# Kernel optimization log

Hardware: AMD Instinct MI355X
Metric: run time of the kernel (lower is better)

## Reference

```python
import jax, jax.numpy as jnp
import numpy as np

S, E, H = 4096, 1024, 16
D = E // H
N_SEG = 64


def setup_inputs() -> dict:
    key = jax.random.key(0)
    ks = jax.random.split(key, 11)
    scale = 0.02
    inp = {
        "x": jax.random.normal(ks[0], (S, E), dtype=jnp.float32),
        "Wq": jax.random.normal(ks[1], (E, E), dtype=jnp.float32) * scale,
        "bq": jax.random.normal(ks[2], (E,), dtype=jnp.float32) * scale,
        "Wk": jax.random.normal(ks[3], (E, E), dtype=jnp.float32) * scale,
        "bk": jax.random.normal(ks[4], (E,), dtype=jnp.float32) * scale,
        "Wv": jax.random.normal(ks[5], (E, E), dtype=jnp.float32) * scale,
        "bv": jax.random.normal(ks[6], (E,), dtype=jnp.float32) * scale,
        "Wo": jax.random.normal(ks[7], (E, E), dtype=jnp.float32) * scale,
        "bo": jax.random.normal(ks[8], (E,), dtype=jnp.float32) * scale,
        "segment_ids": jnp.sort(jax.random.randint(ks[9], (S,), 0, N_SEG)).astype(jnp.int32),
        "pos": 100,
    }
    return inp


def reference(x, Wq, bq, Wk, bk, Wv, bv, Wo, bo, segment_ids, pos):
    # torch Linear: y = x @ W.T + b
    q = (x @ Wq.T + bq).reshape(S, H, D)  # [S, H, D]
    k = (x @ Wk.T + bk).reshape(S, H, D)
    v = (x @ Wv.T + bv).reshape(S, H, D)

    # same-segment mask (contiguous segments from gene-structure dividers)
    mask = segment_ids[:, None] == segment_ids[None, :]  # [S, S]

    # NOTE: original leaves out-of-segment scores at 0 (not -inf) and applies
    # softmax over the FULL row; also no 1/sqrt(d) scaling. Reproduce exactly.
    scores = jnp.einsum("shd,thd->hst", q, k)            # [H, S, S]
    scores = jnp.where(mask[None, :, :], scores, 0.0)
    weights = jax.nn.softmax(scores, axis=-1)            # softmax over full row

    wv = jnp.einsum("hst,thd->shd", weights, v).reshape(S, E)
    out = wv @ Wo.T + bo                                  # [S, E]

    # mean over the main context: tokens sharing pos's segment
    main = (segment_ids == segment_ids[pos]).astype(out.dtype)  # [S]
    result = (out * main[:, None]).sum(axis=0) / main.sum()
    return result
```

## Files before the change

### kernel.cpp

```cpp
#include <hip/hip_runtime.h>
#include <math.h>

#define SS 4096
#define EE 1024
#define HH 16
#define DD 64
#define RMAX 128
#define NCOL 128
#define NTR  8
#define NRED 8
#define NPROJ 768
#define NBG 64
#define NVS 16
#define NATT 256

#define OFF_SUMX  64
#define OFF_BGA   1088
#define OFF_BETA  2112
#define OFF_ALPHA 3136
#define OFF_VSUM  3200
#define OFF_PART  8192
#define OFF_XT    (OFF_PART + EE * NCOL)
#define OFF_QH    (OFF_XT + EE * RMAX)
#define OFF_KTH   (OFF_QH + HH * RMAX * DD)
#define OFF_VH    (OFF_KTH + HH * DD * RMAX)

__device__ __forceinline__ void seg_scan(const int* __restrict__ seg,
                                         const int* __restrict__ posp,
                                         int* sh, int& s0, int& L) {
    if (threadIdx.x == 0) { sh[0] = SS; sh[1] = -1; }
    __syncthreads();
    int sid = seg[posp[0]];
    int lmin = SS, lmax = -1;
    for (int i = threadIdx.x; i < SS; i += 256)
        if (seg[i] == sid) { lmin = min(lmin, i); lmax = max(lmax, i); }
#pragma unroll
    for (int off = 32; off; off >>= 1) {
        lmin = min(lmin, __shfl_xor(lmin, off));
        lmax = max(lmax, __shfl_xor(lmax, off));
    }
    if ((threadIdx.x & 63) == 0) { atomicMin(&sh[0], lmin); atomicMax(&sh[1], lmax); }
    __syncthreads();
    s0 = sh[0];
    L  = sh[1] - sh[0] + 1;
    if (L > RMAX) L = RMAX;
    if (L < 1)    L = 1;
}

__global__ __launch_bounds__(256) void d0_kernel(
    const float* __restrict__ x, const int* __restrict__ seg,
    const int* __restrict__ posp, float* __restrict__ ws) {
    int bid = blockIdx.x, tid = threadIdx.x;
    if (bid < NCOL) {
        float* partT = ws + OFF_PART;
        int r0 = bid * (SS / NCOL);
        const float4* x4 = (const float4*)x;
        float4 a = make_float4(0.f, 0.f, 0.f, 0.f);
#pragma unroll 8
        for (int r = 0; r < SS / NCOL; ++r) {
            float4 v = x4[(size_t)(r0 + r) * 256 + tid];
            a.x += v.x; a.y += v.y; a.z += v.z; a.w += v.w;
        }
        partT[(size_t)(4 * tid + 0) * NCOL + bid] = a.x;
        partT[(size_t)(4 * tid + 1) * NCOL + bid] = a.y;
        partT[(size_t)(4 * tid + 2) * NCOL + bid] = a.z;
        partT[(size_t)(4 * tid + 3) * NCOL + bid] = a.w;
        return;
    }
    __shared__ float t[128 * 129];
    __shared__ int sh[2];
    int s0, L;
    seg_scan(seg, posp, sh, s0, L);
    int kb = bid - NCOL;
    if (kb == 0 && tid == 0) { ((int*)ws)[0] = s0; ((int*)ws)[1] = L; }
    int k0 = kb * 128;
    float* xT = ws + OFF_XT;
    for (int idx = tid; idx < 128 * 32; idx += 256) {
        int r = idx >> 5, c4 = idx & 31;
        float4 v = make_float4(0.f, 0.f, 0.f, 0.f);
        if (r < L) v = *(const float4*)(x + (size_t)(s0 + r) * EE + k0 + c4 * 4);
        t[r * 129 + c4 * 4 + 0] = v.x;
        t[r * 129 + c4 * 4 + 1] = v.y;
        t[r * 129 + c4 * 4 + 2] = v.z;
        t[r * 129 + c4 * 4 + 3] = v.w;
    }
    __syncthreads();
    for (int idx = tid; idx < 128 * 32; idx += 256) {
        int k = idx >> 5, r4 = idx & 31;
        float4 o;
        o.x = t[(r4 * 4 + 0) * 129 + k];
        o.y = t[(r4 * 4 + 1) * 129 + k];
        o.z = t[(r4 * 4 + 2) * 129 + k];
        o.w = t[(r4 * 4 + 3) * 129 + k];
        *(float4*)(xT + (size_t)(k0 + k) * RMAX + r4 * 4) = o;
    }
}

__global__ __launch_bounds__(256) void d1_kernel(
    const float* __restrict__ Wq, const float* __restrict__ bq,
    const float* __restrict__ Wk, const float* __restrict__ bk,
    const float* __restrict__ Wv, const float* __restrict__ bv,
    float* __restrict__ ws) {
    int bid = blockIdx.x, tid = threadIdx.x;
    if (bid < NRED) {
        if (bid == 0) {
            for (int i = tid; i < 1088; i += 256) (ws + OFF_BETA)[i] = 0.f;
        }
        const float* partT = ws + OFF_PART;
        int e  = bid * 128 + (tid >> 1);
        int c0 = (tid & 1) * 64;
        const float4* p4 = (const float4*)(partT + (size_t)e * NCOL + c0);
        float4 s4 = make_float4(0.f, 0.f, 0.f, 0.f);
#pragma unroll
        for (int i = 0; i < 16; ++i) {
            float4 v = p4[i];
            s4.x += v.x; s4.y += v.y; s4.z += v.z; s4.w += v.w;
        }
        float s = s4.x + s4.y + s4.z + s4.w;
        s += __shfl_xor(s, 1);
        if ((tid & 1) == 0) (ws + OFF_SUMX)[e] = s;
        return;
    }
    __shared__ float wsL[4 * EE];
    __shared__ float red[16 * 66];
    int L  = ((const int*)ws)[1];
    int Lp = (L + 63) & ~63;
    int nh = Lp >> 6;
    int pid = bid - NRED;
    int m   = pid >> 8;
    int eb  = pid & 255;
    int e0  = eb * 4;
    const float* W = (m == 0) ? Wq : ((m == 1) ? Wk : Wv);
    const float* b = (m == 0) ? bq : ((m == 1) ? bk : bv);

    {
        const float4* src = (const float4*)(W + (size_t)e0 * EE);
        float4* dst = (float4*)wsL;
#pragma unroll
        for (int i = 0; i < 4; ++i) dst[tid + i * 256] = src[tid + i * 256];
    }
    __syncthreads();

    int lane = tid & 63;
    int w4   = tid >> 6;
    int kbase = w4 * 256;
    const float* x0 = ws + OFF_XT + lane;
    float acc[2][4] = {{0.f, 0.f, 0.f, 0.f}, {0.f, 0.f, 0.f, 0.f}};
    for (int kk = 0; kk < 256; kk += 8) {
        float xv0[8], xv1[8];
#pragma unroll
        for (int u = 0; u < 8; ++u)
            xv0[u] = x0[(size_t)(kbase + kk + u) * RMAX];
        if (nh == 2) {
#pragma unroll
            for (int u = 0; u < 8; ++u)
                xv1[u] = x0[(size_t)(kbase + kk + u) * RMAX + 64];
        }
#pragma unroll
        for (int j = 0; j < 4; ++j) {
            const float4* wp = (const float4*)&wsL[j * EE + kbase + kk];
            float4 wa = wp[0], wb = wp[1];
            acc[0][j] += wa.x * xv0[0] + wa.y * xv0[1] + wa.z * xv0[2] + wa.w * xv0[3]
                       + wb.x * xv0[4] + wb.y * xv0[5] + wb.z * xv0[6] + wb.w * xv0[7];
            if (nh == 2)
                acc[1][j] += wa.x * xv1[0] + wa.y * xv1[1] + wa.z * xv1[2] + wa.w * xv1[3]
                           + wb.x * xv1[4] + wb.y * xv1[5] + wb.z * xv1[6] + wb.w * xv1[7];
        }
    }

    float* qh  = ws + OFF_QH;
    float* kTh = ws + OFF_KTH;
    float* vh  = ws + OFF_VH;
    int h = e0 >> 6;
    for (int h2 = 0; h2 < nh; ++h2) {
        __syncthreads();
#pragma unroll
        for (int j = 0; j < 4; ++j)
            red[(w4 * 4 + j) * 66 + lane] = acc[h2][j];
        __syncthreads();
        int p  = w4;
        int rg = h2 * 64 + lane;
        float v = 0.f;
        if (rg < L)
            v = red[(0 * 4 + p) * 66 + lane] + red[(1 * 4 + p) * 66 + lane]
              + red[(2 * 4 + p) * 66 + lane] + red[(3 * 4 + p) * 66 + lane]
              + b[e0 + p];
        int d0 = (e0 & 63) + p;
        if (m == 1) kTh[(size_t)(h * DD + d0) * RMAX + rg] = v;
        else        ((m == 0) ? qh : vh)[((size_t)h * RMAX + rg) * DD + d0] = v;
    }
}

__global__ __launch_bounds__(256) void d2_kernel(
    const float* __restrict__ Wv, const float* __restrict__ bv,
    float* __restrict__ ws) {
    __shared__ float qS[4 * 64];
    __shared__ float wS[4 * 128];
    __shared__ float vp_[4][64];
    const float* sumx = ws + OFF_SUMX;
    float* bgA    = ws + OFF_BGA;
    float* betap  = ws + OFF_BETA;
    float* alphap = ws + OFF_ALPHA;
    float* vsumh  = ws + OFF_VSUM;
    const float* qh  = ws + OFF_QH;
    const float* kTh = ws + OFF_KTH;
    const float* vh  = ws + OFF_VH;

    int bid = blockIdx.x, tid = threadIdx.x;
    int lane = tid & 63, wave = tid >> 6;
    int L  = ((const int*)ws)[1];
    int Lp = (L + 63) & ~63;

    if (bid < NBG) {
        int e = bid * 16 + (tid >> 4);
        int j = tid & 15;
        const float4* wr  = (const float4*)(Wv + (size_t)e * EE);
        const float4* sx4 = (const float4*)sumx;
        float p = 0.f;
#pragma unroll
        for (int jj = 0; jj < 16; ++jj) {
            float4 w = wr[jj * 16 + j], z = sx4[jj * 16 + j];
            p += w.x * z.x + w.y * z.y + w.z * z.z + w.w * z.w;
        }
        p += __shfl_xor(p, 8);
        p += __shfl_xor(p, 4);
        p += __shfl_xor(p, 2);
        p += __shfl_xor(p, 1);
        if (j == 0) bgA[e] = p + (float)SS * bv[e];
        return;
    }
    if (bid < NBG + NVS) {
        int h = bid - NBG;
        float s = 0.f;
        for (int t = wave; t < Lp; t += 4)
            s += vh[((size_t)h * RMAX + t) * DD + lane];
        vp_[wave][lane] = s;
        __syncthreads();
        if (wave == 0)
            vsumh[h * DD + lane] = vp_[0][lane] + vp_[1][lane]
                                 + vp_[2][lane] + vp_[3][lane];
        return;
    }

    int aid = bid - NBG - NVS;
    int gidbase = aid * 4 + wave;
    int pairs = L * HH;
    float* qSw = qS + wave * 64;
    float* wSw = wS + wave * 128;
    for (int wg = gidbase; wg < pairs; wg += NATT * 4) {
        int h = wg & (HH - 1);
        int r = wg >> 4;
        qSw[lane] = qh[((size_t)h * RMAX + r) * DD + lane];
        float s0 = 0.f, s1 = 0.f;
#pragma unroll
        for (int d = 0; d < 64; ++d) {
            float qd = qSw[d];
            const float* kr = kTh + (size_t)(h * DD + d) * RMAX;
            s0 += qd * kr[lane];
            s1 += qd * kr[64 + lane];
        }
        float v0 = (lane < L)      ? s0 : -3.0e38f;
        float v1 = (64 + lane < L) ? s1 : -3.0e38f;
        float m = fmaxf(0.f, fmaxf(v0, v1));
#pragma unroll
        for (int off = 32; off; off >>= 1) m = fmaxf(m, __shfl_xor(m, off));
        float w0 = (lane < L)      ? __expf(s0 - m) : 0.f;
        float w1 = (64 + lane < L) ? __expf(s1 - m) : 0.f;
        float Zl = w0 + w1;
#pragma unroll
        for (int off = 32; off; off >>= 1) Zl += __shfl_xor(Zl, off);
        float em = __expf(-m);
        float Z  = Zl + (float)(SS - L) * em;
        wSw[lane]      = w0;
        wSw[64 + lane] = w1;
        float acc = 0.f;
#pragma unroll 16
        for (int t = 0; t < Lp; ++t)
            acc += wSw[t] * vh[((size_t)h * RMAX + t) * DD + lane];
        float invZ = 1.0f / Z;
        atomicAdd(&betap[h * DD + lane], acc * invZ);
        if (lane == 0) atomicAdd(&alphap[h], em * invZ);
    }
}

__global__ __launch_bounds__(256) void d3_kernel(
    const float* __restrict__ Wo, const float* __restrict__ bo,
    const float* __restrict__ ws, float* __restrict__ out) {
    __shared__ float z[EE];
    int tid = threadIdx.x;
    int lane = tid & 63, wave = tid >> 6;
    int L = ((const int*)ws)[1];

    {
        int h = tid >> 4;
        float4 beta = ((const float4*)(ws + OFF_BETA))[tid];
        float  a    = (ws + OFF_ALPHA)[h];
        float4 g    = ((const float4*)(ws + OFF_BGA))[tid];
        float4 vs   = ((const float4*)(ws + OFF_VSUM))[tid];
        ((float4*)z)[tid] = make_float4(beta.x + a * (g.x - vs.x),
                                        beta.y + a * (g.y - vs.y),
                                        beta.z + a * (g.z - vs.z),
                                        beta.w + a * (g.w - vs.w));
    }
    __syncthreads();

    int e = blockIdx.x * 4 + wave;
    const float4* wr = (const float4*)(Wo + (size_t)e * EE);
    const float4* z4 = (const float4*)z;
    float p = 0.f;
#pragma unroll
    for (int it = 0; it < 4; ++it) {
        float4 w = wr[it * 64 + lane], zz = z4[it * 64 + lane];
        p += w.x * zz.x + w.y * zz.y + w.z * zz.z + w.w * zz.w;
    }
#pragma unroll
    for (int off = 32; off; off >>= 1) p += __shfl_xor(p, off);
    if (lane == 0) out[e] = bo[e] + p / (float)L;
}

extern "C" void kernel_launch(void* const* d_in, const int* in_sizes, int n_in,
                              void* d_out, int out_size, void* d_ws, size_t ws_size,
                              hipStream_t stream) {
    const float* x   = (const float*)d_in[0];
    const float* Wq  = (const float*)d_in[1];
    const float* bq  = (const float*)d_in[2];
    const float* Wk  = (const float*)d_in[3];
    const float* bk  = (const float*)d_in[4];
    const float* Wv  = (const float*)d_in[5];
    const float* bv  = (const float*)d_in[6];
    const float* Wo  = (const float*)d_in[7];
    const float* bo  = (const float*)d_in[8];
    const int*   seg = (const int*)d_in[9];
    const int*   pos = (const int*)d_in[10];
    float*       out = (float*)d_out;
    float*       ws  = (float*)d_ws;

    d0_kernel<<<NCOL + NTR, 256, 0, stream>>>(x, seg, pos, ws);
    d1_kernel<<<NRED + NPROJ, 256, 0, stream>>>(Wq, bq, Wk, bk, Wv, bv, ws);
    d2_kernel<<<NBG + NVS + NATT, 256, 0, stream>>>(Wv, bv, ws);
    d3_kernel<<<EE / 4, 256, 0, stream>>>(Wo, bo, ws, out);
}
```

Baseline: 71.57 us.

## Tile QKV projection over rows/cols with split-K partials and separate reduce kernel

Drops the separate transpose of the main-segment rows of x. The QKV projection kernel now loads x rows and W tiles straight into shared memory, computing 64-row by 32-column tiles split four ways over K, and writes partial sums to workspace. A new d1b kernel adds the four partials plus bias and scatters the results into the per-head q, kT and v layouts. This trades the old per-block full-K reduction and x-transpose pass for more parallel blocks and smaller W tiles, at the cost of an extra kernel launch and a round trip of the partial sums through global memory.

```diff
diff --git a/kernel.cpp b/kernel.cpp
--- a/kernel.cpp
+++ b/kernel.cpp
@@ -7,9 +7,9 @@
 #define DD 64
 #define RMAX 128
 #define NCOL 128
-#define NTR  8
 #define NRED 8
 #define NPROJ 768
+#define NREDB 96
 #define NBG 64
 #define NVS 16
 #define NATT 256
@@ -20,10 +20,10 @@
 #define OFF_ALPHA 3136
 #define OFF_VSUM  3200
 #define OFF_PART  8192
-#define OFF_XT    (OFF_PART + EE * NCOL)
-#define OFF_QH    (OFF_XT + EE * RMAX)
+#define OFF_QH    270336
 #define OFF_KTH   (OFF_QH + HH * RMAX * DD)
 #define OFF_VH    (OFF_KTH + HH * DD * RMAX)
+#define OFF_YP    (OFF_VH + HH * RMAX * DD)
 
 __device__ __forceinline__ void seg_scan(const int* __restrict__ seg,
                                          const int* __restrict__ posp,
@@ -67,40 +67,16 @@
         partT[(size_t)(4 * tid + 3) * NCOL + bid] = a.w;
         return;
     }
-    __shared__ float t[128 * 129];
     __shared__ int sh[2];
     int s0, L;
     seg_scan(seg, posp, sh, s0, L);
-    int kb = bid - NCOL;
-    if (kb == 0 && tid == 0) { ((int*)ws)[0] = s0; ((int*)ws)[1] = L; }
-    int k0 = kb * 128;
-    float* xT = ws + OFF_XT;
-    for (int idx = tid; idx < 128 * 32; idx += 256) {
-        int r = idx >> 5, c4 = idx & 31;
-        float4 v = make_float4(0.f, 0.f, 0.f, 0.f);
-        if (r < L) v = *(const float4*)(x + (size_t)(s0 + r) * EE + k0 + c4 * 4);
-        t[r * 129 + c4 * 4 + 0] = v.x;
-        t[r * 129 + c4 * 4 + 1] = v.y;
-        t[r * 129 + c4 * 4 + 2] = v.z;
-        t[r * 129 + c4 * 4 + 3] = v.w;
-    }
-    __syncthreads();
-    for (int idx = tid; idx < 128 * 32; idx += 256) {
-        int k = idx >> 5, r4 = idx & 31;
-        float4 o;
-        o.x = t[(r4 * 4 + 0) * 129 + k];
-        o.y = t[(r4 * 4 + 1) * 129 + k];
-        o.z = t[(r4 * 4 + 2) * 129 + k];
-        o.w = t[(r4 * 4 + 3) * 129 + k];
-        *(float4*)(xT + (size_t)(k0 + k) * RMAX + r4 * 4) = o;
-    }
+    if (tid == 0) { ((int*)ws)[0] = s0; ((int*)ws)[1] = L; }
 }
 
 __global__ __launch_bounds__(256) void d1_kernel(
-    const float* __restrict__ Wq, const float* __restrict__ bq,
-    const float* __restrict__ Wk, const float* __restrict__ bk,
-    const float* __restrict__ Wv, const float* __restrict__ bv,
-    float* __restrict__ ws) {
+    const float* __restrict__ x,
+    const float* __restrict__ Wq, const float* __restrict__ Wk,
+    const float* __restrict__ Wv, float* __restrict__ ws) {
     int bid = blockIdx.x, tid = threadIdx.x;
     if (bid < NRED) {
         if (bid == 0) {
@@ -121,73 +97,110 @@
         if ((tid & 1) == 0) (ws + OFF_SUMX)[e] = s;
         return;
     }
-    __shared__ float wsL[4 * EE];
-    __shared__ float red[16 * 66];
+    __shared__ float xs[64 * 130];
+    __shared__ float wsm[128 * 36];
+    int s0 = ((const int*)ws)[0];
     int L  = ((const int*)ws)[1];
     int Lp = (L + 63) & ~63;
-    int nh = Lp >> 6;
     int pid = bid - NRED;
-    int m   = pid >> 8;
-    int eb  = pid & 255;
-    int e0  = eb * 4;
+    int rt  = (pid >= 384) ? 1 : 0;
+    int rem = pid - rt * 384;
+    int m   = rem >> 7;
+    int rem2 = rem & 127;
+    int kc  = rem2 >> 5;
+    int et  = rem2 & 31;
+    int r0  = rt * 64;
+    if (r0 >= Lp) return;
     const float* W = (m == 0) ? Wq : ((m == 1) ? Wk : Wv);
-    const float* b = (m == 0) ? bq : ((m == 1) ? bk : bv);
-
-    {
-        const float4* src = (const float4*)(W + (size_t)e0 * EE);
-        float4* dst = (float4*)wsL;
-#pragma unroll
-        for (int i = 0; i < 4; ++i) dst[tid + i * 256] = src[tid + i * 256];
-    }
-    __syncthreads();
-
+    int e0t = et * 32;
     int lane = tid & 63;
     int w4   = tid >> 6;
-    int kbase = w4 * 256;
-    const float* x0 = ws + OFF_XT + lane;
-    float acc[2][4] = {{0.f, 0.f, 0.f, 0.f}, {0.f, 0.f, 0.f, 0.f}};
-    for (int kk = 0; kk < 256; kk += 8) {
-        float xv0[8], xv1[8];
-#pragma unroll
-        for (int u = 0; u < 8; ++u)
-            xv0[u] = x0[(size_t)(kbase + kk + u) * RMAX];
-        if (nh == 2) {
-#pragma unroll
-            for (int u = 0; u < 8; ++u)
-                xv1[u] = x0[(size_t)(kbase + kk + u) * RMAX + 64];
-        }
-#pragma unroll
-        for (int j = 0; j < 4; ++j) {
-            const float4* wp = (const float4*)&wsL[j * EE + kbase + kk];
-            float4 wa = wp[0], wb = wp[1];
-            acc[0][j] += wa.x * xv0[0] + wa.y * xv0[1] + wa.z * xv0[2] + wa.w * xv0[3]
-                       + wb.x * xv0[4] + wb.y * xv0[5] + wb.z * xv0[6] + wb.w * xv0[7];
-            if (nh == 2)
-                acc[1][j] += wa.x * xv1[0] + wa.y * xv1[1] + wa.z * xv1[2] + wa.w * xv1[3]
-                           + wb.x * xv1[4] + wb.y * xv1[5] + wb.z * xv1[6] + wb.w * xv1[7];
-        }
-    }
-
+    int eo   = w4 * 8;
+    float a0 = 0.f, a1 = 0.f, a2 = 0.f, a3 = 0.f;
+    float a4 = 0.f, a5 = 0.f, a6 = 0.f, a7 = 0.f;
+
+    for (int rr = 0; rr < 2; ++rr) {
+        int k0 = kc * 256 + rr * 128;
+        __syncthreads();
+        for (int idx = tid; idx < 2048; idx += 256) {
+            int k4 = idx & 31, r = idx >> 5;
+            float4 v = make_float4(0.f, 0.f, 0.f, 0.f);
+            if (r0 + r < L)
+                v = *(const float4*)(x + (size_t)(s0 + r0 + r) * EE + k0 + k4 * 4);
+            int kb = k4 * 2;
+            xs[(kb + 0) * 130 + r * 2 + 0] = v.x;
+            xs[(kb + 0) * 130 + r * 2 + 1] = v.y;
+            xs[(kb + 1) * 130 + r * 2 + 0] = v.z;
+            xs[(kb + 1) * 130 + r * 2 + 1] = v.w;
+        }
+        for (int idx = tid; idx < 1024; idx += 256) {
+            int k4 = idx & 31, e = idx >> 5;
+            float4 v = *(const float4*)(W + (size_t)(e0t + e) * EE + k0 + k4 * 4);
+            wsm[(k4 * 4 + 0) * 36 + e] = v.x;
+            wsm[(k4 * 4 + 1) * 36 + e] = v.y;
+            wsm[(k4 * 4 + 2) * 36 + e] = v.z;
+            wsm[(k4 * 4 + 3) * 36 + e] = v.w;
+        }
+        __syncthreads();
+#pragma unroll 8
+        for (int k2 = 0; k2 < 64; ++k2) {
+            float2 xr = *(const float2*)&xs[k2 * 130 + lane * 2];
+            const float4* wA = (const float4*)&wsm[(2 * k2 + 0) * 36 + eo];
+            const float4* wB = (const float4*)&wsm[(2 * k2 + 1) * 36 + eo];
+            float4 wa0 = wA[0], wa1 = wA[1];
+            float4 wb0 = wB[0], wb1 = wB[1];
+            a0 += wa0.x * xr.x + wb0.x * xr.y;
+            a1 += wa0.y * xr.x + wb0.y * xr.y;
+            a2 += wa0.z * xr.x + wb0.z * xr.y;
+            a3 += wa0.w * xr.x + wb0.w * xr.y;
+            a4 += wa1.x * xr.x + wb1.x * xr.y;
+            a5 += wa1.y * xr.x + wb1.y * xr.y;
+            a6 += wa1.z * xr.x + wb1.z * xr.y;
+            a7 += wa1.w * xr.x + wb1.w * xr.y;
+        }
+    }
+    float* dst = ws + OFF_YP + ((size_t)(m * 4 + kc) * RMAX + (r0 + lane)) * EE
+               + e0t + eo;
+    *(float4*)(dst)     = make_float4(a0, a1, a2, a3);
+    *(float4*)(dst + 4) = make_float4(a4, a5, a6, a7);
+}
+
+__global__ __launch_bounds__(256) void d1b_kernel(
+    const float* __restrict__ bq, const float* __restrict__ bk,
+    const float* __restrict__ bv, float* __restrict__ ws) {
+    int bid = blockIdx.x, tid = threadIdx.x;
+    int L = ((const int*)ws)[1];
+    int m  = bid / 32;
+    int rg = bid % 32;
+    const float* b = (m == 0) ? bq : ((m == 1) ? bk : bv);
     float* qh  = ws + OFF_QH;
     float* kTh = ws + OFF_KTH;
     float* vh  = ws + OFF_VH;
-    int h = e0 >> 6;
-    for (int h2 = 0; h2 < nh; ++h2) {
-        __syncthreads();
-#pragma unroll
-        for (int j = 0; j < 4; ++j)
-            red[(w4 * 4 + j) * 66 + lane] = acc[h2][j];
-        __syncthreads();
-        int p  = w4;
-        int rg = h2 * 64 + lane;
-        float v = 0.f;
-        if (rg < L)
-            v = red[(0 * 4 + p) * 66 + lane] + red[(1 * 4 + p) * 66 + lane]
-              + red[(2 * 4 + p) * 66 + lane] + red[(3 * 4 + p) * 66 + lane]
-              + b[e0 + p];
-        int d0 = (e0 & 63) + p;
-        if (m == 1) kTh[(size_t)(h * DD + d0) * RMAX + rg] = v;
-        else        ((m == 0) ? qh : vh)[((size_t)h * RMAX + rg) * DD + d0] = v;
+    float4 bb = ((const float4*)b)[tid];
+    int e = tid * 4;
+    int h = e >> 6, d = e & 63;
+#pragma unroll
+    for (int rr = 0; rr < 4; ++rr) {
+        int r = rg * 4 + rr;
+        const float4* y0 = (const float4*)(ws + OFF_YP + ((size_t)(m * 4 + 0) * RMAX + r) * EE);
+        const float4* y1 = (const float4*)(ws + OFF_YP + ((size_t)(m * 4 + 1) * RMAX + r) * EE);
+        const float4* y2 = (const float4*)(ws + OFF_YP + ((size_t)(m * 4 + 2) * RMAX + r) * EE);
+        const float4* y3 = (const float4*)(ws + OFF_YP + ((size_t)(m * 4 + 3) * RMAX + r) * EE);
+        float4 s0 = y0[tid], s1 = y1[tid], s2 = y2[tid], s3 = y3[tid];
+        float o0 = s0.x + s1.x + s2.x + s3.x + bb.x;
+        float o1 = s0.y + s1.y + s2.y + s3.y + bb.y;
+        float o2 = s0.z + s1.z + s2.z + s3.z + bb.z;
+        float o3 = s0.w + s1.w + s2.w + s3.w + bb.w;
+        if (r >= L) { o0 = 0.f; o1 = 0.f; o2 = 0.f; o3 = 0.f; }
+        if (m == 1) {
+            kTh[(size_t)(h * DD + d + 0) * RMAX + r] = o0;
+            kTh[(size_t)(h * DD + d + 1) * RMAX + r] = o1;
+            kTh[(size_t)(h * DD + d + 2) * RMAX + r] = o2;
+            kTh[(size_t)(h * DD + d + 3) * RMAX + r] = o3;
+        } else {
+            float* y = (m == 0) ? qh : vh;
+            *(float4*)&y[((size_t)h * RMAX + r) * DD + d] = make_float4(o0, o1, o2, o3);
+        }
     }
 }
 
@@ -335,8 +348,9 @@
     float*       out = (float*)d_out;
     float*       ws  = (float*)d_ws;
 
-    d0_kernel<<<NCOL + NTR, 256, 0, stream>>>(x, seg, pos, ws);
-    d1_kernel<<<NRED + NPROJ, 256, 0, stream>>>(Wq, bq, Wk, bk, Wv, bv, ws);
+    d0_kernel<<<NCOL + 1, 256, 0, stream>>>(x, seg, pos, ws);
+    d1_kernel<<<NRED + NPROJ, 256, 0, stream>>>(x, Wq, Wk, Wv, ws);
+    d1b_kernel<<<NREDB, 256, 0, stream>>>(bq, bk, bv, ws);
     d2_kernel<<<NBG + NVS + NATT, 256, 0, stream>>>(Wv, bv, ws);
     d3_kernel<<<EE / 4, 256, 0, stream>>>(Wo, bo, ws, out);
 }
```

Measured after the change: 71.50 us. No clear change (-0.1%).

## Drop x transpose stage; project QKV with register-held weight rows and shuffle reduction

Applied to the files above, without the earlier changes.

Removes the d0 transpose blocks that wrote a transposed copy of the main-segment rows of x into workspace. The QKV projection now keeps each output column's weight row in registers, split across 32 lanes, and streams x rows straight from global memory. Each row's dot product is reduced with wavefront shuffles, and the next row is double-buffered in registers. This cuts the transpose pass, the workspace round-trip and the LDS staging, at the cost of a serial per-row shuffle reduction and only 384 projection blocks.

```diff
diff --git a/kernel.cpp b/kernel.cpp
--- a/kernel.cpp
+++ b/kernel.cpp
@@ -7,9 +7,8 @@
 #define DD 64
 #define RMAX 128
 #define NCOL 128
-#define NTR  8
 #define NRED 8
-#define NPROJ 768
+#define NPROJ 384
 #define NBG 64
 #define NVS 16
 #define NATT 256
@@ -20,8 +19,7 @@
 #define OFF_ALPHA 3136
 #define OFF_VSUM  3200
 #define OFF_PART  8192
-#define OFF_XT    (OFF_PART + EE * NCOL)
-#define OFF_QH    (OFF_XT + EE * RMAX)
+#define OFF_QH    270336
 #define OFF_KTH   (OFF_QH + HH * RMAX * DD)
 #define OFF_VH    (OFF_KTH + HH * DD * RMAX)
 
@@ -67,36 +65,14 @@
         partT[(size_t)(4 * tid + 3) * NCOL + bid] = a.w;
         return;
     }
-    __shared__ float t[128 * 129];
     __shared__ int sh[2];
     int s0, L;
     seg_scan(seg, posp, sh, s0, L);
-    int kb = bid - NCOL;
-    if (kb == 0 && tid == 0) { ((int*)ws)[0] = s0; ((int*)ws)[1] = L; }
-    int k0 = kb * 128;
-    float* xT = ws + OFF_XT;
-    for (int idx = tid; idx < 128 * 32; idx += 256) {
-        int r = idx >> 5, c4 = idx & 31;
-        float4 v = make_float4(0.f, 0.f, 0.f, 0.f);
-        if (r < L) v = *(const float4*)(x + (size_t)(s0 + r) * EE + k0 + c4 * 4);
-        t[r * 129 + c4 * 4 + 0] = v.x;
-        t[r * 129 + c4 * 4 + 1] = v.y;
-        t[r * 129 + c4 * 4 + 2] = v.z;
-        t[r * 129 + c4 * 4 + 3] = v.w;
-    }
-    __syncthreads();
-    for (int idx = tid; idx < 128 * 32; idx += 256) {
-        int k = idx >> 5, r4 = idx & 31;
-        float4 o;
-        o.x = t[(r4 * 4 + 0) * 129 + k];
-        o.y = t[(r4 * 4 + 1) * 129 + k];
-        o.z = t[(r4 * 4 + 2) * 129 + k];
-        o.w = t[(r4 * 4 + 3) * 129 + k];
-        *(float4*)(xT + (size_t)(k0 + k) * RMAX + r4 * 4) = o;
-    }
+    if (tid == 0) { ((int*)ws)[0] = s0; ((int*)ws)[1] = L; }
 }
 
 __global__ __launch_bounds__(256) void d1_kernel(
+    const float* __restrict__ x,
     const float* __restrict__ Wq, const float* __restrict__ bq,
     const float* __restrict__ Wk, const float* __restrict__ bk,
     const float* __restrict__ Wv, const float* __restrict__ bv,
@@ -121,74 +97,71 @@
         if ((tid & 1) == 0) (ws + OFF_SUMX)[e] = s;
         return;
     }
-    __shared__ float wsL[4 * EE];
-    __shared__ float red[16 * 66];
+    int s0 = ((const int*)ws)[0];
     int L  = ((const int*)ws)[1];
     int Lp = (L + 63) & ~63;
-    int nh = Lp >> 6;
-    int pid = bid - NRED;
-    int m   = pid >> 8;
-    int eb  = pid & 255;
-    int e0  = eb * 4;
-    const float* W = (m == 0) ? Wq : ((m == 1) ? Wk : Wv);
-    const float* b = (m == 0) ? bq : ((m == 1) ? bk : bv);
-
-    {
-        const float4* src = (const float4*)(W + (size_t)e0 * EE);
-        float4* dst = (float4*)wsL;
-#pragma unroll
-        for (int i = 0; i < 4; ++i) dst[tid + i * 256] = src[tid + i * 256];
-    }
-    __syncthreads();
-
+    int pid  = bid - NRED;
     int lane = tid & 63;
     int w4   = tid >> 6;
-    int kbase = w4 * 256;
-    const float* x0 = ws + OFF_XT + lane;
-    float acc[2][4] = {{0.f, 0.f, 0.f, 0.f}, {0.f, 0.f, 0.f, 0.f}};
-    for (int kk = 0; kk < 256; kk += 8) {
-        float xv0[8], xv1[8];
-#pragma unroll
-        for (int u = 0; u < 8; ++u)
-            xv0[u] = x0[(size_t)(kbase + kk + u) * RMAX];
-        if (nh == 2) {
-#pragma unroll
-            for (int u = 0; u < 8; ++u)
-                xv1[u] = x0[(size_t)(kbase + kk + u) * RMAX + 64];
-        }
-#pragma unroll
-        for (int j = 0; j < 4; ++j) {
-            const float4* wp = (const float4*)&wsL[j * EE + kbase + kk];
-            float4 wa = wp[0], wb = wp[1];
-            acc[0][j] += wa.x * xv0[0] + wa.y * xv0[1] + wa.z * xv0[2] + wa.w * xv0[3]
-                       + wb.x * xv0[4] + wb.y * xv0[5] + wb.z * xv0[6] + wb.w * xv0[7];
-            if (nh == 2)
-                acc[1][j] += wa.x * xv1[0] + wa.y * xv1[1] + wa.z * xv1[2] + wa.w * xv1[3]
-                           + wb.x * xv1[4] + wb.y * xv1[5] + wb.z * xv1[6] + wb.w * xv1[7];
-        }
-    }
-
+    int e2   = lane >> 5;
+    int kg   = lane & 31;
+    int ge   = pid * 8 + w4 * 2 + e2;
+    int m    = ge >> 10;
+    int em   = ge & 1023;
+    const float* Wm = (m == 0) ? Wq : ((m == 1) ? Wk : Wv);
+    const float* bm = (m == 0) ? bq : ((m == 1) ? bk : bv);
+    float bias = bm[em];
+    const float4* wp = (const float4*)(Wm + (size_t)em * EE + kg * 32);
+    float4 w0 = wp[0], w1 = wp[1], w2 = wp[2], w3 = wp[3];
+    float4 w4v = wp[4], w5 = wp[5], w6 = wp[6], w7 = wp[7];
+    int h = em >> 6, d = em & 63;
     float* qh  = ws + OFF_QH;
     float* kTh = ws + OFF_KTH;
     float* vh  = ws + OFF_VH;
-    int h = e0 >> 6;
-    for (int h2 = 0; h2 < nh; ++h2) {
-        __syncthreads();
-#pragma unroll
-        for (int j = 0; j < 4; ++j)
-            red[(w4 * 4 + j) * 66 + lane] = acc[h2][j];
-        __syncthreads();
-        int p  = w4;
-        int rg = h2 * 64 + lane;
-        float v = 0.f;
-        if (rg < L)
-            v = red[(0 * 4 + p) * 66 + lane] + red[(1 * 4 + p) * 66 + lane]
-              + red[(2 * 4 + p) * 66 + lane] + red[(3 * 4 + p) * 66 + lane]
-              + b[e0 + p];
-        int d0 = (e0 & 63) + p;
-        if (m == 1) kTh[(size_t)(h * DD + d0) * RMAX + rg] = v;
-        else        ((m == 0) ? qh : vh)[((size_t)h * RMAX + rg) * DD + d0] = v;
-    }
+    int r0off = pid & (Lp - 1);
+
+#define LOADX(A0,A1,A2,A3,A4,A5,A6,A7, RR)                                   \
+    {                                                                         \
+        int r_  = (r0off + (RR)) & (Lp - 1);                                  \
+        int rx_ = (r_ < L) ? (s0 + r_) : s0;                                  \
+        const float4* xp_ = (const float4*)(x + (size_t)rx_ * EE + kg * 32);  \
+        A0 = xp_[0]; A1 = xp_[1]; A2 = xp_[2]; A3 = xp_[3];                   \
+        A4 = xp_[4]; A5 = xp_[5]; A6 = xp_[6]; A7 = xp_[7];                   \
+    }
+#define BODY(A0,A1,A2,A3,A4,A5,A6,A7, RR)                                    \
+    {                                                                         \
+        float t = A0.x * w0.x + A0.y * w0.y + A0.z * w0.z + A0.w * w0.w;      \
+        t += A1.x * w1.x + A1.y * w1.y + A1.z * w1.z + A1.w * w1.w;           \
+        t += A2.x * w2.x + A2.y * w2.y + A2.z * w2.z + A2.w * w2.w;           \
+        t += A3.x * w3.x + A3.y * w3.y + A3.z * w3.z + A3.w * w3.w;           \
+        t += A4.x * w4v.x + A4.y * w4v.y + A4.z * w4v.z + A4.w * w4v.w;       \
+        t += A5.x * w5.x + A5.y * w5.y + A5.z * w5.z + A5.w * w5.w;           \
+        t += A6.x * w6.x + A6.y * w6.y + A6.z * w6.z + A6.w * w6.w;           \
+        t += A7.x * w7.x + A7.y * w7.y + A7.z * w7.z + A7.w * w7.w;           \
+        t += __shfl_xor(t, 16);                                               \
+        t += __shfl_xor(t, 8);                                                \
+        t += __shfl_xor(t, 4);                                                \
+        t += __shfl_xor(t, 2);                                                \
+        t += __shfl_xor(t, 1);                                                \
+        if (kg == 0) {                                                        \
+            int r_ = (r0off + (RR)) & (Lp - 1);                               \
+            float v_ = (r_ < L) ? (t + bias) : 0.f;                           \
+            if (m == 1) kTh[(size_t)(h * DD + d) * RMAX + r_] = v_;           \
+            else ((m == 0) ? qh : vh)[((size_t)h * RMAX + r_) * DD + d] = v_; \
+        }                                                                     \
+    }
+
+    float4 a0, a1, a2, a3, a4, a5, a6, a7;
+    float4 b0, b1, b2, b3, b4, b5, b6, b7;
+    LOADX(a0,a1,a2,a3,a4,a5,a6,a7, 0)
+    for (int rr = 0; rr < Lp; rr += 2) {
+        LOADX(b0,b1,b2,b3,b4,b5,b6,b7, rr + 1)
+        BODY(a0,a1,a2,a3,a4,a5,a6,a7, rr)
+        LOADX(a0,a1,a2,a3,a4,a5,a6,a7, rr + 2)
+        BODY(b0,b1,b2,b3,b4,b5,b6,b7, rr + 1)
+    }
+#undef LOADX
+#undef BODY
 }
 
 __global__ __launch_bounds__(256) void d2_kernel(
@@ -335,8 +308,8 @@
     float*       out = (float*)d_out;
     float*       ws  = (float*)d_ws;
 
-    d0_kernel<<<NCOL + NTR, 256, 0, stream>>>(x, seg, pos, ws);
-    d1_kernel<<<NRED + NPROJ, 256, 0, stream>>>(Wq, bq, Wk, bk, Wv, bv, ws);
+    d0_kernel<<<NCOL + 1, 256, 0, stream>>>(x, seg, pos, ws);
+    d1_kernel<<<NRED + NPROJ, 256, 0, stream>>>(x, Wq, bq, Wk, bk, Wv, bv, ws);
     d2_kernel<<<NBG + NVS + NATT, 256, 0, stream>>>(Wv, bv, ws);
     d3_kernel<<<EE / 4, 256, 0, stream>>>(Wo, bo, ws, out);
 }
```

Result: slower. 264.6 us (+269.8%).
